# Kernel optimization log

Measured on AMD Instinct MI355X. Metric: run time of the kernel, lower is better.

Reference implementation:

```python
import jax, jax.numpy as jnp
import numpy as np

K = 100
TEMPERATURE = 0.1


def setup_inputs() -> dict:
    key = jax.random.key(0)
    k1, k2 = jax.random.split(key)
    x = jax.random.normal(k1, (8, 128, 60, 60), dtype=jnp.float32)
    W = jax.random.normal(k2, (128, 2 * K), dtype=jnp.float32) * 0.02  # torch Linear(k*2, d_model).weight
    b = jnp.zeros((128,), dtype=jnp.float32)
    return {"x": x, "W": W, "b": b}


def reference(x, W, b):
    x0, x1 = jnp.split(x, 2, axis=0)
    n, c, h, w = x0.shape
    hw = h * w
    # n c h w -> n (h w) c
    f0 = jnp.transpose(x0.reshape(n, c, hw), (0, 2, 1))
    f1 = jnp.transpose(x1.reshape(n, c, hw), (0, 2, 1))
    # (f0/sqrt(c)) @ (f1/sqrt(c))^T / T  ==  f0 @ f1^T / (c*T)
    sm = jnp.einsum('nld,nsd->nls', f0, f1) / (c * TEMPERATURE)
    cm = (jax.nn.softmax(sm, axis=1) * jax.nn.softmax(sm, axis=2)).reshape(n, hw * hw)
    _, topi = jax.lax.top_k(cm, K)  # (n, K)
    qindex = topi // hw
    rindex = topi % hw
    coords0 = jnp.stack([qindex % w, qindex // w], axis=-1).astype(jnp.float32) / w  # (n, K, 2) as (x, y)
    coords1 = jnp.stack([rindex % w, rindex // w], axis=-1).astype(jnp.float32) / w
    # create_meshgrid(h, w, normalized=False): (1, h*w, 2) with (x, y), row-major
    gy, gx = jnp.meshgrid(jnp.arange(h), jnp.arange(w), indexing='ij')
    grid = jnp.stack([gx, gy], axis=-1).reshape(1, hw, 2).astype(jnp.float32) / w
    offsets0 = grid[:, :, None, :] - coords0[:, None, :, :]  # (n, hw, K, 2)
    offsets1 = grid[:, :, None, :] - coords1[:, None, :, :]
    emb0 = offsets0.reshape(n, hw, 2 * K) @ W.T + b  # (n, hw, d_model)
    emb1 = offsets1.reshape(n, hw, 2 * K) @ W.T + b
    f0 = f0 + emb0
    f1 = f1 + emb1
    f = jnp.concatenate([f0, f1], axis=0)  # (2n, hw, d)
    # n (h w) d -> n d h w
    return jnp.transpose(f, (0, 2, 1)).reshape(2 * n, c, h, w)
```

## Files before the change

kernel.cpp:

```cpp
#include <hip/hip_runtime.h>

#define HW 3600
#define PADR 3712
#define NF4 900
#define CAP 16384
#define KSEL 100
#define NT 58
typedef unsigned long long U64;

using short8   = __attribute__((ext_vector_type(8))) short;
using float4v  = __attribute__((ext_vector_type(4))) float;
using float16v = __attribute__((ext_vector_type(16))) float;

__device__ __forceinline__ unsigned monof(float f) {
    unsigned b = __float_as_uint(f);
    return (b & 0x80000000u) ? ~b : (b | 0x80000000u);
}
__device__ __forceinline__ float unmonof(unsigned m) {
    return __uint_as_float((m & 0x80000000u) ? (m ^ 0x80000000u) : ~m);
}
__device__ __forceinline__ unsigned short f2bf(float f) {
    unsigned b = __float_as_uint(f);
    return (unsigned short)((b + 0x7FFFu + ((b >> 16) & 1u)) >> 16);
}
__device__ __forceinline__ float bf2f(unsigned short h) {
    return __uint_as_float(((unsigned)h) << 16);
}
__device__ __forceinline__ void async16(const void* g, void* l) {
    __builtin_amdgcn_global_load_lds((const __attribute__((address_space(1))) void*)g,
                                     (__attribute__((address_space(3))) void*)l, 16, 0, 0);
}


__global__ __launch_bounds__(256) void conv_k(
    const float* __restrict__ x,
    unsigned short* __restrict__ hiT, unsigned short* __restrict__ loT)
{
    int b = blockIdx.z, l0 = blockIdx.x * 64, d0 = blockIdx.y * 64;
    __shared__ float t[64][65];
    int tid = threadIdx.x;
#pragma unroll
    for (int r = 0; r < 4; r++) {
        int idx = tid + 256 * r;
        int d = idx >> 4, lq = idx & 15;
        int l = l0 + lq * 4;
        const float* src = x + ((size_t)b * 128 + d0 + d) * HW;
        float4 v;
        if (l + 3 < HW) v = *(const float4*)(src + l);
        else {
            v.x = (l     < HW) ? src[l]     : 0.f;
            v.y = (l + 1 < HW) ? src[l + 1] : 0.f;
            v.z = (l + 2 < HW) ? src[l + 2] : 0.f;
            v.w = (l + 3 < HW) ? src[l + 3] : 0.f;
        }
        t[lq * 4 + 0][d] = v.x; t[lq * 4 + 1][d] = v.y;
        t[lq * 4 + 2][d] = v.z; t[lq * 4 + 3][d] = v.w;
    }
    __syncthreads();
    const int rblk = l0 >> 7;
#pragma unroll
    for (int r = 0; r < 2; r++) {
        int idx = tid + 256 * r;
        int l = idx & 63, dq = idx >> 6;
        unsigned hp[4], lp[4];
#pragma unroll
        for (int j = 0; j < 4; j++) {
            float f0 = t[l][dq * 8 + 2 * j], f1 = t[l][dq * 8 + 2 * j + 1];
            unsigned short h0 = f2bf(f0), h1 = f2bf(f1);
            unsigned short g0 = f2bf(f0 - bf2f(h0)), g1 = f2bf(f1 - bf2f(h1));
            hp[j] = (unsigned)h0 | ((unsigned)h1 << 16);
            lp[j] = (unsigned)g0 | ((unsigned)g1 << 16);
        }
        size_t o = ((size_t)(b * 29 + rblk) * 16 + (d0 >> 3) + dq) * 1024
                 + (size_t)((l0 + l) & 127) * 8;
        *(uint4*)(hiT + o) = make_uint4(hp[0], hp[1], hp[2], hp[3]);
        *(uint4*)(loT + o) = make_uint4(lp[0], lp[1], lp[2], lp[3]);
    }
}

__global__ __launch_bounds__(256) void gemm_mfma_k(
    const unsigned short* __restrict__ hiT, const unsigned short* __restrict__ loT,
    float* __restrict__ den_row, float* __restrict__ den_col,
    float* __restrict__ maxvt)
{
    const int batch = blockIdx.z, bx = blockIdx.x, by = blockIdx.y;
    __shared__ __align__(16) unsigned char smem[34816];
    unsigned short (*stage)[4][128][8] = (unsigned short (*)[4][128][8])smem;

    const int tid = threadIdx.x;
    const int lane = tid & 63, w = tid >> 6;
    const int wr = w >> 1, wc = w & 1;
    const int l31 = lane & 31, h = lane >> 5;

    const unsigned short* psrc = (w == 0) ? hiT : (w == 1) ? loT : (w == 2) ? hiT : loT;
    const int bsel = (w < 2) ? batch : batch + 4;
    const int rblk = (w < 2) ? by : bx;
    const size_t cbase = ((size_t)(bsel * 29 + rblk) * 16) * 1024;

    float16v acc[2][2];
#pragma unroll
    for (int i = 0; i < 2; i++)
#pragma unroll
        for (int j = 0; j < 2; j++) acc[i][j] = (float16v)(0.f);

    for (int k0 = 0; k0 < 128; k0 += 32) {
#pragma unroll
        for (int i = 0; i < 8; i++) {
            int kb = i >> 1, half = i & 1;
            const unsigned short* g = psrc + cbase + (size_t)((k0 >> 3) + kb) * 1024
                                    + (half << 9) + lane * 8;
            async16(g, &stage[w][kb][half << 6][0]);
        }
        __syncthreads();
#pragma unroll
        for (int j = 0; j < 2; j++) {
            int kb = j * 2 + h;
            short8 ah[2], al[2], bh[2], bl[2];
#pragma unroll
            for (int t = 0; t < 2; t++) {
                ah[t] = *(const short8*)&stage[0][kb][wr * 64 + t * 32 + l31][0];
                al[t] = *(const short8*)&stage[1][kb][wr * 64 + t * 32 + l31][0];
                bh[t] = *(const short8*)&stage[2][kb][wc * 64 + t * 32 + l31][0];
                bl[t] = *(const short8*)&stage[3][kb][wc * 64 + t * 32 + l31][0];
            }
#pragma unroll
            for (int mt = 0; mt < 2; mt++)
#pragma unroll
                for (int nt = 0; nt < 2; nt++) {
                    acc[mt][nt] = __builtin_amdgcn_mfma_f32_32x32x16_bf16(ah[mt], bh[nt], acc[mt][nt], 0, 0, 0);
                    acc[mt][nt] = __builtin_amdgcn_mfma_f32_32x32x16_bf16(ah[mt], bl[nt], acc[mt][nt], 0, 0, 0);
                    acc[mt][nt] = __builtin_amdgcn_mfma_f32_32x32x16_bf16(al[mt], bh[nt], acc[mt][nt], 0, 0, 0);
                }
        }
        __syncthreads();
    }

    const float scale = 0.078125f;
    float* T = ((float*)smem) + w * (64 * 34);
    const bool interior = (bx < 28) && (by < 28);
    const int col0 = bx * 128 + wc * 64 + l31;
    const bool c0v = interior || (col0 < HW);
    const bool c1v = interior || (col0 + 32 < HW);
    float cs0 = 0.f, cs1 = 0.f;

#pragma unroll
    for (int mt = 0; mt < 2; mt++)
#pragma unroll
        for (int reg = 0; reg < 16; reg++) {
            float v0 = acc[mt][0][reg] * scale;
            float v1 = acc[mt][1][reg] * scale;
            float e0 = c0v ? __expf(v0) : 0.f;
            float e1 = c1v ? __expf(v1) : 0.f;
            int row64 = mt * 32 + (reg & 3) + 8 * (reg >> 2) + 4 * h;
            bool rv = interior || (by * 128 + wr * 64 + row64 < HW);
            if (rv) { cs0 += e0; cs1 += e1; }
            T[row64 * 34 + l31] = e0 + e1;
        }
    __asm__ __volatile__("s_waitcnt lgkmcnt(0)" ::: "memory");
    float rsum = 0.f;
#pragma unroll
    for (int i = 0; i < 16; i++) {
        float2 p = *(const float2*)&T[lane * 34 + 2 * i];
        rsum += p.x + p.y;
    }
    __asm__ __volatile__("s_waitcnt lgkmcnt(0)" ::: "memory");
    const int lrow = by * 128 + wr * 64 + lane;
    const bool rowv = interior || (lrow < HW);
    if (rowv) atomicAdd(&den_row[(size_t)batch * HW + lrow], rsum);

#pragma unroll
    for (int mt = 0; mt < 2; mt++)
#pragma unroll
        for (int reg = 0; reg < 16; reg++) {
            float m0 = c0v ? acc[mt][0][reg] : -3.4e38f;
            float m1 = c1v ? acc[mt][1][reg] : -3.4e38f;
            int row64 = mt * 32 + (reg & 3) + 8 * (reg >> 2) + 4 * h;
            T[row64 * 34 + l31] = fmaxf(m0, m1) * scale;
        }
    __asm__ __volatile__("s_waitcnt lgkmcnt(0)" ::: "memory");
    float rmax = -3.4e38f;
#pragma unroll
    for (int i = 0; i < 16; i++) {
        float2 p = *(const float2*)&T[lane * 34 + 2 * i];
        rmax = fmaxf(rmax, fmaxf(p.x, p.y));
    }
    const int ct = bx * 2 + wc;
    if (rowv) maxvt[((size_t)batch * NT + ct) * PADR + lrow] = rmax;

    cs0 += __shfl_xor(cs0, 32);
    cs1 += __shfl_xor(cs1, 32);
    if (h == 0) {
        if (c0v) atomicAdd(&den_col[(size_t)batch * HW + col0], cs0);
        if (c1v) atomicAdd(&den_col[(size_t)batch * HW + col0 + 32], cs1);
    }
}

__global__ __launch_bounds__(256) void stat_k(
    const float* __restrict__ den_row, const float* __restrict__ den_col,
    const float* __restrict__ maxvt, float* __restrict__ keylb)
{
    const int b = blockIdx.z, tid = threadIdx.x;
    __shared__ float lncS[HW];
    __shared__ float mlsS[NT];
    for (int i = tid; i < HW; i += 256)
        lncS[i] = __logf(den_col[(size_t)b * HW + i]);
    __syncthreads();
    if (tid < NT) {
        float mx = -3.4e38f;
        int s0 = tid * 64, s1 = s0 + 64; if (s1 > HW) s1 = HW;
        for (int s = s0; s < s1; s++) mx = fmaxf(mx, lncS[s]);
        if (s0 >= HW) mx = 1e30f;
        mlsS[tid] = mx;
    }
    __syncthreads();
    int j = blockIdx.x * 240 + tid;
    if (tid < 240 && j < HW) {
        float best = -3.4e38f;
#pragma unroll 2
        for (int t = 0; t < NT; t++)
            best = fmaxf(best, 2.0f * maxvt[((size_t)b * NT + t) * PADR + j] - mlsS[t]);
        keylb[(size_t)b * HW + j] = best - __logf(den_row[(size_t)b * HW + j]);
    }
}

__global__ __launch_bounds__(256) void tau_k(
    const float* __restrict__ keylb, float* __restrict__ tau)
{
    const int b = blockIdx.z, tid = threadIdx.x;
    __shared__ unsigned keyS[HW];
    __shared__ unsigned hist[4096];
    __shared__ unsigned pc[256];
    __shared__ int b1S, c1S, b2S, lcnt;
    __shared__ unsigned bestS;
    __shared__ unsigned list[1024];

    for (int i = tid; i < 4096; i += 256) hist[i] = 0u;
    if (tid == 0) { lcnt = 0; bestS = 0u; }
    __syncthreads();
    for (int i = tid; i < HW; i += 256) {
        unsigned k = monof(keylb[(size_t)b * HW + i]);
        keyS[i] = k;
        atomicAdd(&hist[k >> 20], 1u);
    }
    __syncthreads();
    { unsigned s = 0; for (int j = 0; j < 16; j++) s += hist[tid * 16 + j]; pc[tid] = s; }
    __syncthreads();
    if (tid == 0) {
        unsigned cum = 0; int cs_ = 255;
        for (; cs_ > 0; cs_--) { if (cum + pc[cs_] >= (unsigned)KSEL) break; cum += pc[cs_]; }
        int bb = cs_ * 16 + 15;
        for (; bb > cs_ * 16; bb--) { if (cum + hist[bb] >= (unsigned)KSEL) break; cum += hist[bb]; }
        b1S = bb; c1S = (int)cum;
    }
    __syncthreads();
    int b1 = b1S;
    for (int i = tid; i < 4096; i += 256) hist[i] = 0u;
    __syncthreads();
    for (int i = tid; i < HW; i += 256) {
        unsigned k = keyS[i];
        if ((int)(k >> 20) == b1) atomicAdd(&hist[(k >> 8) & 4095], 1u);
    }
    __syncthreads();
    { unsigned s = 0; for (int j = 0; j < 16; j++) s += hist[tid * 16 + j]; pc[tid] = s; }
    __syncthreads();
    if (tid == 0) {
        unsigned cum = (unsigned)c1S; int cs_ = 255;
        for (; cs_ > 0; cs_--) { if (cum + pc[cs_] >= (unsigned)KSEL) break; cum += pc[cs_]; }
        int bb = cs_ * 16 + 15;
        for (; bb > cs_ * 16; bb--) { if (cum + hist[bb] >= (unsigned)KSEL) break; cum += hist[bb]; }
        b2S = bb;
    }
    __syncthreads();
    int b2 = b2S;
    for (int i = tid; i < HW; i += 256) {
        unsigned k = keyS[i]; int hb = (int)(k >> 20);
        if (hb > b1 || (hb == b1 && (int)((k >> 8) & 4095) >= b2)) {
            int p = atomicAdd(&lcnt, 1);
            if (p < 1024) list[p] = k;
        }
    }
    __syncthreads();
    int L = lcnt; if (L > 1024) L = 1024;
    for (int i = tid; i < L; i += 256) {
        unsigned e = list[i]; int c = 0;
        for (int j = 0; j < L; j++) c += (list[j] >= e) ? 1 : 0;
        if (c >= KSEL) atomicMax(&bestS, e);
    }
    __syncthreads();
    if (tid == 0) tau[b] = unmonof(bestS) - 3e-4f;
}

__global__ __launch_bounds__(256) void recollect_k(
    const unsigned short* __restrict__ hiT, const unsigned short* __restrict__ loT,
    const float* __restrict__ den_row, const float* __restrict__ den_col,
    const float* __restrict__ maxvt, const float* __restrict__ tau,
    uint2* __restrict__ cand, int* __restrict__ cnt)
{
    const int t = blockIdx.x, batch = blockIdx.y;
    const int tid = threadIdx.x;
    __shared__ float lnrS[HW];
    __shared__ float lncS[64];
    __shared__ int prS[HW];
    __shared__ int pcS;
    __shared__ float mnlS;

    if (tid < 64) {
        int c = t * 64 + tid;
        float lc = (c < HW) ? __logf(den_col[(size_t)batch * HW + c]) : 1e30f;
        lncS[tid] = lc;
        float mn = lc;
#pragma unroll
        for (int off = 1; off < 64; off <<= 1) mn = fminf(mn, __shfl_xor(mn, off));
        if (tid == 0) mnlS = mn;
    }
    for (int r = tid; r < HW; r += 256)
        lnrS[r] = __logf(den_row[(size_t)batch * HW + r]);
    if (tid == 0) pcS = 0;
    __syncthreads();

    const float tv = tau[batch];
    const float tvm = tv - 3e-4f;
    const float mnl = mnlS;
    const float* mv = maxvt + ((size_t)batch * NT + t) * PADR;
    for (int r = tid; r < HW; r += 256) {
        float bnd = 2.0f * mv[r] - lnrS[r] - mnl;
        if (bnd >= tvm) {
            int p = atomicAdd(&pcS, 1);
            prS[p] = r;
        }
    }
    __syncthreads();
    const int pc = pcS;
    if (pc == 0) return;

    const unsigned short* Ah = hiT + 0;
    const unsigned short* Al = loT + 0;
    const int lane = tid & 63, w = tid >> 6;
    const int m = lane & 15, q = lane >> 4;
    const float scale = 0.078125f;
    const size_t abase = (size_t)batch * PADR * 128;
    const size_t bbase = (size_t)(batch + 4) * PADR * 128;

    for (int g = w; g * 16 < pc; g += 4) {
        int pi = g * 16 + m;
        int rowv = (pi < pc) ? prS[pi] : HW;
        float ldrv = (pi < pc) ? lnrS[rowv] : 0.f;
        size_t arow = abase + ((size_t)(rowv >> 7) * 16) * 1024 + (size_t)(rowv & 127) * 8;

        float4v acc[4];
#pragma unroll
        for (int i = 0; i < 4; i++) acc[i] = (float4v){0.f, 0.f, 0.f, 0.f};
#pragma unroll
        for (int k0 = 0; k0 < 128; k0 += 32) {
            int kb = (k0 >> 3) + q;
            short8 ah = *(const short8*)(Ah + arow + (size_t)kb * 1024);
            short8 al = *(const short8*)(Al + arow + (size_t)kb * 1024);
#pragma unroll
            for (int nt = 0; nt < 4; nt++) {
                int c = t * 64 + nt * 16 + m;
                size_t brow = bbase + ((size_t)(c >> 7) * 16 + kb) * 1024 + (size_t)(c & 127) * 8;
                short8 bh = *(const short8*)(hiT + brow);
                short8 bl = *(const short8*)(loT + brow);
                acc[nt] = __builtin_amdgcn_mfma_f32_16x16x32_bf16(ah, bh, acc[nt], 0, 0, 0);
                acc[nt] = __builtin_amdgcn_mfma_f32_16x16x32_bf16(ah, bl, acc[nt], 0, 0, 0);
                acc[nt] = __builtin_amdgcn_mfma_f32_16x16x32_bf16(al, bh, acc[nt], 0, 0, 0);
            }
        }
#pragma unroll
        for (int nt = 0; nt < 4; nt++) {
            int c = t * 64 + nt * 16 + m;
            if (c >= HW) continue;
            float ldc = lncS[nt * 16 + m];
#pragma unroll
            for (int r = 0; r < 4; r++) {
                int ri = q * 4 + r;
                if (g * 16 + ri >= pc) continue;
                int rowo = __shfl(rowv, ri);
                float ldro = __shfl(ldrv, ri);
                float v = acc[nt][r] * scale;
                float tt = 2.0f * v - ldro - ldc;
                if (tt >= tv) {
                    int p = atomicAdd(&cnt[batch], 1);
                    if (p < CAP)
                        cand[(size_t)batch * CAP + p] =
                            make_uint2(monof(tt), (unsigned)(rowo * HW + c));
                }
            }
        }
    }
}

__global__ __launch_bounds__(256) void select_k(
    const uint2* __restrict__ cand, const int* __restrict__ cnt,
    const float* __restrict__ W,
    float* __restrict__ C0, float* __restrict__ C1,
    float* __restrict__ Sx, float* __restrict__ Sy)
{
    const int batch = blockIdx.z, tid = threadIdx.x;
    const uint2* cb = cand + (size_t)batch * CAP;
    int M = cnt[batch]; if (M > CAP) M = CAP;

    __shared__ unsigned hist[4096];
    __shared__ unsigned pc[256];
    __shared__ int b1S, c1S, b2S, lcnt;
    __shared__ U64 list[512];
    __shared__ int topiS[KSEL];
    __shared__ float cx0S[KSEL], cy0S[KSEL], cx1S[KSEL], cy1S[KSEL];

    for (int i = tid; i < 4096; i += 256) hist[i] = 0u;
    if (tid == 0) lcnt = 0;
    __syncthreads();
    for (int i = tid; i < M; i += 256) atomicAdd(&hist[cb[i].x >> 20], 1u);
    __syncthreads();
    { unsigned s = 0; for (int j = 0; j < 16; j++) s += hist[tid * 16 + j]; pc[tid] = s; }
    __syncthreads();
    if (tid == 0) {
        unsigned cum = 0; int cs_ = 255;
        for (; cs_ > 0; cs_--) { if (cum + pc[cs_] >= (unsigned)KSEL) break; cum += pc[cs_]; }
        int bb = cs_ * 16 + 15;
        for (; bb > cs_ * 16; bb--) { if (cum + hist[bb] >= (unsigned)KSEL) break; cum += hist[bb]; }
        b1S = bb; c1S = (int)cum;
    }
    __syncthreads();
    int b1 = b1S;
    for (int i = tid; i < 4096; i += 256) hist[i] = 0u;
    __syncthreads();
    for (int i = tid; i < M; i += 256) {
        unsigned k = cb[i].x;
        if ((int)(k >> 20) == b1) atomicAdd(&hist[(k >> 8) & 4095], 1u);
    }
    __syncthreads();
    { unsigned s = 0; for (int j = 0; j < 16; j++) s += hist[tid * 16 + j]; pc[tid] = s; }
    __syncthreads();
    if (tid == 0) {
        unsigned cum = (unsigned)c1S; int cs_ = 255;
        for (; cs_ > 0; cs_--) { if (cum + pc[cs_] >= (unsigned)KSEL) break; cum += pc[cs_]; }
        int bb = cs_ * 16 + 15;
        for (; bb > cs_ * 16; bb--) { if (cum + hist[bb] >= (unsigned)KSEL) break; cum += hist[bb]; }
        b2S = bb;
    }
    __syncthreads();
    int b2 = b2S;
    for (int i = tid; i < M; i += 256) {
        uint2 e = cb[i];
        int hb = (int)(e.x >> 20);
        if (hb > b1 || (hb == b1 && (int)((e.x >> 8) & 4095) >= b2)) {
            int p = atomicAdd(&lcnt, 1);
            if (p < 512) list[p] = ((U64)e.x << 32) | (unsigned)(~e.y);
        }
    }
    __syncthreads();
    int L = lcnt; if (L > 512) L = 512;
    for (int i = tid; i < L; i += 256) {
        U64 e = list[i]; int r = 0;
        for (int j = 0; j < L; j++) r += (list[j] > e) ? 1 : 0;
        if (r < KSEL) topiS[r] = (int)(~(unsigned)(e & 0xffffffffu));
    }
    __syncthreads();

    if (tid < KSEL) {
        int idx = topiS[tid];
        int qq = idx / HW, rr = idx - qq * HW;
        cx0S[tid] = (float)(qq % 60) / 60.0f;
        cy0S[tid] = (float)(qq / 60) / 60.0f;
        cx1S[tid] = (float)(rr % 60) / 60.0f;
        cy1S[tid] = (float)(rr / 60) / 60.0f;
    }
    __syncthreads();
    if (tid < 128) {
        const float* wr_ = W + tid * 200;
        float c0 = 0.f, c1 = 0.f, sx = 0.f, sy = 0.f;
        for (int k = 0; k < KSEL; k++) {
            float wx = wr_[2 * k], wy = wr_[2 * k + 1];
            c0 += cx0S[k] * wx + cy0S[k] * wy;
            c1 += cx1S[k] * wx + cy1S[k] * wy;
            sx += wx; sy += wy;
        }
        C0[batch * 128 + tid] = c0;
        C1[batch * 128 + tid] = c1;
        if (batch == 0) { Sx[tid] = sx; Sy[tid] = sy; }
    }
}

__global__ __launch_bounds__(256) void final_k(
    const float* __restrict__ x, const float* __restrict__ bias,
    const float* __restrict__ C0, const float* __restrict__ C1,
    const float* __restrict__ Sx, const float* __restrict__ Sy,
    float* __restrict__ out)
{
    int bd = blockIdx.x;
    int b = bd >> 7, d = bd & 127;
    float cst = bias[d] - ((b < 4) ? C0[b * 128 + d] : C1[(b - 4) * 128 + d]);
    float sx = Sx[d], sy = Sy[d];
    const float4* xin = (const float4*)(x + (size_t)bd * HW);
    float4* o4 = (float4*)(out + (size_t)bd * HW);
    for (int f = threadIdx.x; f < NF4; f += 256) {
        float4 v = xin[f];
        int p0 = f * 4;
        float gy = (float)(p0 / 60) / 60.0f;
        float gxb = (float)(p0 % 60);
        float add = cst + gy * sy;
        v.x += add + ((gxb       ) / 60.0f) * sx;
        v.y += add + ((gxb + 1.f) / 60.0f) * sx;
        v.z += add + ((gxb + 2.f) / 60.0f) * sx;
        v.w += add + ((gxb + 3.f) / 60.0f) * sx;
        o4[f] = v;
    }
}

extern "C" void kernel_launch(void* const* d_in, const int* in_sizes, int n_in,
                              void* d_out, int out_size, void* d_ws, size_t ws_size,
                              hipStream_t stream)
{
    const float* x    = (const float*)d_in[0];
    const float* W    = (const float*)d_in[1];
    const float* bias = (const float*)d_in[2];
    float* out = (float*)d_out;

    char* ws = (char*)d_ws;
    float*    den_row = (float*)(ws + 0);
    float*    den_col = (float*)(ws + 57600);
    int*      cnt     = (int*)  (ws + 115200);
    float*    tau     = (float*)(ws + 115216);
    float*    keylb   = (float*)(ws + 115264);
    float*    C0      = (float*)(ws + 172864);
    float*    C1      = (float*)(ws + 174912);
    float*    Sx      = (float*)(ws + 176960);
    float*    Sy      = (float*)(ws + 177472);
    uint2*    cand    = (uint2*)(ws + 178048);
    float*    maxvt   = (float*)(ws + 702336);
    unsigned short* hiT = (unsigned short*)(ws + 4147072);
    unsigned short* loT = (unsigned short*)(ws + 11749248);

    hipMemsetAsync(ws, 0, 115232, stream);

    conv_k     <<<dim3(58, 2, 8),  256, 0, stream>>>(x, hiT, loT);
    gemm_mfma_k<<<dim3(29, 29, 4), 256, 0, stream>>>(hiT, loT, den_row, den_col, maxvt);
    stat_k     <<<dim3(15, 1, 4),  256, 0, stream>>>(den_row, den_col, maxvt, keylb);
    tau_k      <<<dim3(1, 1, 4),   256, 0, stream>>>(keylb, tau);
    recollect_k<<<dim3(NT, 4),     256, 0, stream>>>(hiT, loT, den_row, den_col, maxvt, tau, cand, cnt);
    select_k   <<<dim3(1, 1, 4),   256, 0, stream>>>(cand, cnt, W, C0, C1, Sx, Sy);
    final_k    <<<dim3(1024),      256, 0, stream>>>(x, bias, C0, C1, Sx, Sy, out);
}
```

Measured before the change: 229.9 us.

## Fuse stat/tau/select kernels, double-buffer GEMM stages, drop memset

The memset is replaced by zeroing the denominators inside conv_k. The GEMM now double-buffers its async LDS staging, waiting on vmcnt so the next k-slice loads while MFMAs run on the current one. The stat and tau computation is folded into every recollect_k block, each writing per-tile candidate slices without global atomics. Top-k selection plus the W projection are merged into final_k, which every output block recomputes redundantly. This cuts launches and serialized single-block kernels, at the cost of repeated threshold and top-k work per block and a 6144-entry candidate cap.

```diff
diff --git a/kernel.cpp b/kernel.cpp
--- a/kernel.cpp
+++ b/kernel.cpp
@@ -3,7 +3,7 @@
 #define HW 3600
 #define PADR 3712
 #define NF4 900
-#define CAP 16384
+#define SLICE 2048
 #define KSEL 100
 #define NT 58
 typedef unsigned long long U64;
@@ -34,11 +34,19 @@
 
 __global__ __launch_bounds__(256) void conv_k(
     const float* __restrict__ x,
-    unsigned short* __restrict__ hiT, unsigned short* __restrict__ loT)
+    unsigned short* __restrict__ hiT, unsigned short* __restrict__ loT,
+    float* __restrict__ den)
 {
     int b = blockIdx.z, l0 = blockIdx.x * 64, d0 = blockIdx.y * 64;
     __shared__ float t[64][65];
     int tid = threadIdx.x;
+    if (blockIdx.y == 0 && blockIdx.z == 0) {
+        int base = blockIdx.x * 512;
+        for (int i = tid; i < 512; i += 256) {
+            int g = base + i;
+            if (g < 28800) den[g] = 0.f;
+        }
+    }
 #pragma unroll
     for (int r = 0; r < 4; r++) {
         int idx = tid + 256 * r;
@@ -84,8 +92,7 @@
     float* __restrict__ maxvt)
 {
     const int batch = blockIdx.z, bx = blockIdx.x, by = blockIdx.y;
-    __shared__ __align__(16) unsigned char smem[34816];
-    unsigned short (*stage)[4][128][8] = (unsigned short (*)[4][128][8])smem;
+    __shared__ __align__(16) unsigned short stage[2][4][4][128][8];
 
     const int tid = threadIdx.x;
     const int lane = tid & 63, w = tid >> 6;
@@ -97,31 +104,43 @@
     const int rblk = (w < 2) ? by : bx;
     const size_t cbase = ((size_t)(bsel * 29 + rblk) * 16) * 1024;
 
-    float16v acc[2][2];
-#pragma unroll
-    for (int i = 0; i < 2; i++)
-#pragma unroll
-        for (int j = 0; j < 2; j++) acc[i][j] = (float16v)(0.f);
-
-    for (int k0 = 0; k0 < 128; k0 += 32) {
+    auto issue = [&](int buf, int k0) {
 #pragma unroll
         for (int i = 0; i < 8; i++) {
             int kb = i >> 1, half = i & 1;
             const unsigned short* g = psrc + cbase + (size_t)((k0 >> 3) + kb) * 1024
                                     + (half << 9) + lane * 8;
-            async16(g, &stage[w][kb][half << 6][0]);
-        }
-        __syncthreads();
+            async16(g, &stage[buf][w][kb][half << 6][0]);
+        }
+    };
+
+    float16v acc[2][2];
+#pragma unroll
+    for (int i = 0; i < 2; i++)
+#pragma unroll
+        for (int j = 0; j < 2; j++) acc[i][j] = (float16v)(0.f);
+
+    issue(0, 0);
+#pragma unroll
+    for (int it = 0; it < 4; it++) {
+        if (it < 3) {
+            issue((it + 1) & 1, (it + 1) * 32);
+            __asm__ __volatile__("s_waitcnt vmcnt(8)" ::: "memory");
+        } else {
+            __asm__ __volatile__("s_waitcnt vmcnt(0)" ::: "memory");
+        }
+        __asm__ __volatile__("s_barrier" ::: "memory");
+        const int cb = it & 1;
 #pragma unroll
         for (int j = 0; j < 2; j++) {
             int kb = j * 2 + h;
             short8 ah[2], al[2], bh[2], bl[2];
 #pragma unroll
             for (int t = 0; t < 2; t++) {
-                ah[t] = *(const short8*)&stage[0][kb][wr * 64 + t * 32 + l31][0];
-                al[t] = *(const short8*)&stage[1][kb][wr * 64 + t * 32 + l31][0];
-                bh[t] = *(const short8*)&stage[2][kb][wc * 64 + t * 32 + l31][0];
-                bl[t] = *(const short8*)&stage[3][kb][wc * 64 + t * 32 + l31][0];
+                ah[t] = *(const short8*)&stage[cb][0][kb][wr * 64 + t * 32 + l31][0];
+                al[t] = *(const short8*)&stage[cb][1][kb][wr * 64 + t * 32 + l31][0];
+                bh[t] = *(const short8*)&stage[cb][2][kb][wc * 64 + t * 32 + l31][0];
+                bl[t] = *(const short8*)&stage[cb][3][kb][wc * 64 + t * 32 + l31][0];
             }
 #pragma unroll
             for (int mt = 0; mt < 2; mt++)
@@ -132,11 +151,12 @@
                     acc[mt][nt] = __builtin_amdgcn_mfma_f32_32x32x16_bf16(al[mt], bh[nt], acc[mt][nt], 0, 0, 0);
                 }
         }
-        __syncthreads();
-    }
+        __asm__ __volatile__("s_barrier" ::: "memory");
+    }
+    __syncthreads();
 
     const float scale = 0.078125f;
-    float* T = ((float*)smem) + w * (64 * 34);
+    float* T = ((float*)stage) + w * (64 * 34);
     const bool interior = (bx < 28) && (by < 28);
     const int col0 = bx * 128 + wc * 64 + l31;
     const bool c0v = interior || (col0 < HW);
@@ -195,115 +215,33 @@
     }
 }
 
-__global__ __launch_bounds__(256) void stat_k(
-    const float* __restrict__ den_row, const float* __restrict__ den_col,
-    const float* __restrict__ maxvt, float* __restrict__ keylb)
-{
-    const int b = blockIdx.z, tid = threadIdx.x;
-    __shared__ float lncS[HW];
-    __shared__ float mlsS[NT];
-    for (int i = tid; i < HW; i += 256)
-        lncS[i] = __logf(den_col[(size_t)b * HW + i]);
-    __syncthreads();
-    if (tid < NT) {
-        float mx = -3.4e38f;
-        int s0 = tid * 64, s1 = s0 + 64; if (s1 > HW) s1 = HW;
-        for (int s = s0; s < s1; s++) mx = fmaxf(mx, lncS[s]);
-        if (s0 >= HW) mx = 1e30f;
-        mlsS[tid] = mx;
-    }
-    __syncthreads();
-    int j = blockIdx.x * 240 + tid;
-    if (tid < 240 && j < HW) {
-        float best = -3.4e38f;
-#pragma unroll 2
-        for (int t = 0; t < NT; t++)
-            best = fmaxf(best, 2.0f * maxvt[((size_t)b * NT + t) * PADR + j] - mlsS[t]);
-        keylb[(size_t)b * HW + j] = best - __logf(den_row[(size_t)b * HW + j]);
-    }
-}
-
-__global__ __launch_bounds__(256) void tau_k(
-    const float* __restrict__ keylb, float* __restrict__ tau)
-{
-    const int b = blockIdx.z, tid = threadIdx.x;
-    __shared__ unsigned keyS[HW];
-    __shared__ unsigned hist[4096];
-    __shared__ unsigned pc[256];
-    __shared__ int b1S, c1S, b2S, lcnt;
-    __shared__ unsigned bestS;
-    __shared__ unsigned list[1024];
-
-    for (int i = tid; i < 4096; i += 256) hist[i] = 0u;
-    if (tid == 0) { lcnt = 0; bestS = 0u; }
-    __syncthreads();
-    for (int i = tid; i < HW; i += 256) {
-        unsigned k = monof(keylb[(size_t)b * HW + i]);
-        keyS[i] = k;
-        atomicAdd(&hist[k >> 20], 1u);
-    }
-    __syncthreads();
-    { unsigned s = 0; for (int j = 0; j < 16; j++) s += hist[tid * 16 + j]; pc[tid] = s; }
-    __syncthreads();
-    if (tid == 0) {
-        unsigned cum = 0; int cs_ = 255;
-        for (; cs_ > 0; cs_--) { if (cum + pc[cs_] >= (unsigned)KSEL) break; cum += pc[cs_]; }
-        int bb = cs_ * 16 + 15;
-        for (; bb > cs_ * 16; bb--) { if (cum + hist[bb] >= (unsigned)KSEL) break; cum += hist[bb]; }
-        b1S = bb; c1S = (int)cum;
-    }
-    __syncthreads();
-    int b1 = b1S;
-    for (int i = tid; i < 4096; i += 256) hist[i] = 0u;
-    __syncthreads();
-    for (int i = tid; i < HW; i += 256) {
-        unsigned k = keyS[i];
-        if ((int)(k >> 20) == b1) atomicAdd(&hist[(k >> 8) & 4095], 1u);
-    }
-    __syncthreads();
-    { unsigned s = 0; for (int j = 0; j < 16; j++) s += hist[tid * 16 + j]; pc[tid] = s; }
-    __syncthreads();
-    if (tid == 0) {
-        unsigned cum = (unsigned)c1S; int cs_ = 255;
-        for (; cs_ > 0; cs_--) { if (cum + pc[cs_] >= (unsigned)KSEL) break; cum += pc[cs_]; }
-        int bb = cs_ * 16 + 15;
-        for (; bb > cs_ * 16; bb--) { if (cum + hist[bb] >= (unsigned)KSEL) break; cum += hist[bb]; }
-        b2S = bb;
-    }
-    __syncthreads();
-    int b2 = b2S;
-    for (int i = tid; i < HW; i += 256) {
-        unsigned k = keyS[i]; int hb = (int)(k >> 20);
-        if (hb > b1 || (hb == b1 && (int)((k >> 8) & 4095) >= b2)) {
-            int p = atomicAdd(&lcnt, 1);
-            if (p < 1024) list[p] = k;
-        }
-    }
-    __syncthreads();
-    int L = lcnt; if (L > 1024) L = 1024;
-    for (int i = tid; i < L; i += 256) {
-        unsigned e = list[i]; int c = 0;
-        for (int j = 0; j < L; j++) c += (list[j] >= e) ? 1 : 0;
-        if (c >= KSEL) atomicMax(&bestS, e);
-    }
-    __syncthreads();
-    if (tid == 0) tau[b] = unmonof(bestS) - 3e-4f;
-}
-
 __global__ __launch_bounds__(256) void recollect_k(
     const unsigned short* __restrict__ hiT, const unsigned short* __restrict__ loT,
     const float* __restrict__ den_row, const float* __restrict__ den_col,
-    const float* __restrict__ maxvt, const float* __restrict__ tau,
-    uint2* __restrict__ cand, int* __restrict__ cnt)
+    const float* __restrict__ maxvt,
+    uint2* __restrict__ cand, int* __restrict__ cnt58)
 {
     const int t = blockIdx.x, batch = blockIdx.y;
     const int tid = threadIdx.x;
     __shared__ float lnrS[HW];
+    __shared__ float maxlncS[NT];
     __shared__ float lncS[64];
-    __shared__ int prS[HW];
-    __shared__ int pcS;
-    __shared__ float mnlS;
-
+    __shared__ float mnlS, tauS;
+    __shared__ unsigned uS[HW];
+    __shared__ unsigned hist[4096];
+    __shared__ unsigned hpc[256];
+    __shared__ int b1S, c1S, b2S, lcntS, pcS, ccS;
+    __shared__ unsigned bestS;
+    __shared__ unsigned listS[1024];
+
+    for (int i = tid; i < HW; i += 256)
+        lnrS[i] = __logf(den_row[(size_t)batch * HW + i]);
+    if (tid < NT) {
+        float mx = -3.4e38f;
+        int s0 = tid * 64, s1 = s0 + 64; if (s1 > HW) s1 = HW;
+        for (int s = s0; s < s1; s++) mx = fmaxf(mx, __logf(den_col[(size_t)batch * HW + s]));
+        maxlncS[tid] = (s0 < HW) ? mx : 1e30f;
+    }
     if (tid < 64) {
         int c = t * 64 + tid;
         float lc = (c < HW) ? __logf(den_col[(size_t)batch * HW + c]) : 1e30f;
@@ -313,12 +251,67 @@
         for (int off = 1; off < 64; off <<= 1) mn = fminf(mn, __shfl_xor(mn, off));
         if (tid == 0) mnlS = mn;
     }
-    for (int r = tid; r < HW; r += 256)
-        lnrS[r] = __logf(den_row[(size_t)batch * HW + r]);
-    if (tid == 0) pcS = 0;
-    __syncthreads();
-
-    const float tv = tau[batch];
+    for (int i = tid; i < 4096; i += 256) hist[i] = 0u;
+    if (tid == 0) { lcntS = 0; bestS = 0u; pcS = 0; ccS = 0; }
+    __syncthreads();
+
+    for (int r = tid; r < HW; r += 256) {
+        float best = -3.4e38f;
+        for (int tt = 0; tt < NT; tt++)
+            best = fmaxf(best, 2.0f * maxvt[((size_t)batch * NT + tt) * PADR + r] - maxlncS[tt]);
+        unsigned k = monof(best - lnrS[r]);
+        uS[r] = k;
+        atomicAdd(&hist[k >> 20], 1u);
+    }
+    __syncthreads();
+    { unsigned s = 0; for (int j = 0; j < 16; j++) s += hist[tid * 16 + j]; hpc[tid] = s; }
+    __syncthreads();
+    if (tid == 0) {
+        unsigned cum = 0; int cs_ = 255;
+        for (; cs_ > 0; cs_--) { if (cum + hpc[cs_] >= (unsigned)KSEL) break; cum += hpc[cs_]; }
+        int bb = cs_ * 16 + 15;
+        for (; bb > cs_ * 16; bb--) { if (cum + hist[bb] >= (unsigned)KSEL) break; cum += hist[bb]; }
+        b1S = bb; c1S = (int)cum;
+    }
+    __syncthreads();
+    int b1 = b1S;
+    for (int i = tid; i < 4096; i += 256) hist[i] = 0u;
+    __syncthreads();
+    for (int i = tid; i < HW; i += 256) {
+        unsigned k = uS[i];
+        if ((int)(k >> 20) == b1) atomicAdd(&hist[(k >> 8) & 4095], 1u);
+    }
+    __syncthreads();
+    { unsigned s = 0; for (int j = 0; j < 16; j++) s += hist[tid * 16 + j]; hpc[tid] = s; }
+    __syncthreads();
+    if (tid == 0) {
+        unsigned cum = (unsigned)c1S; int cs_ = 255;
+        for (; cs_ > 0; cs_--) { if (cum + hpc[cs_] >= (unsigned)KSEL) break; cum += hpc[cs_]; }
+        int bb = cs_ * 16 + 15;
+        for (; bb > cs_ * 16; bb--) { if (cum + hist[bb] >= (unsigned)KSEL) break; cum += hist[bb]; }
+        b2S = bb;
+    }
+    __syncthreads();
+    int b2 = b2S;
+    for (int i = tid; i < HW; i += 256) {
+        unsigned k = uS[i]; int hb = (int)(k >> 20);
+        if (hb > b1 || (hb == b1 && (int)((k >> 8) & 4095) >= b2)) {
+            int p = atomicAdd(&lcntS, 1);
+            if (p < 1024) listS[p] = k;
+        }
+    }
+    __syncthreads();
+    int L = lcntS; if (L > 1024) L = 1024;
+    for (int i = tid; i < L; i += 256) {
+        unsigned e = listS[i]; int c = 0;
+        for (int j = 0; j < L; j++) c += (listS[j] >= e) ? 1 : 0;
+        if (c >= KSEL) atomicMax(&bestS, e);
+    }
+    __syncthreads();
+    if (tid == 0) tauS = unmonof(bestS) - 3e-4f;
+    __syncthreads();
+
+    const float tv = tauS;
     const float tvm = tv - 3e-4f;
     const float mnl = mnlS;
     const float* mv = maxvt + ((size_t)batch * NT + t) * PADR;
@@ -326,175 +319,153 @@
         float bnd = 2.0f * mv[r] - lnrS[r] - mnl;
         if (bnd >= tvm) {
             int p = atomicAdd(&pcS, 1);
-            prS[p] = r;
+            ((int*)uS)[p] = r;
         }
     }
     __syncthreads();
     const int pc = pcS;
-    if (pc == 0) return;
-
-    const unsigned short* Ah = hiT + 0;
-    const unsigned short* Al = loT + 0;
-    const int lane = tid & 63, w = tid >> 6;
-    const int m = lane & 15, q = lane >> 4;
-    const float scale = 0.078125f;
-    const size_t abase = (size_t)batch * PADR * 128;
-    const size_t bbase = (size_t)(batch + 4) * PADR * 128;
-
-    for (int g = w; g * 16 < pc; g += 4) {
-        int pi = g * 16 + m;
-        int rowv = (pi < pc) ? prS[pi] : HW;
-        float ldrv = (pi < pc) ? lnrS[rowv] : 0.f;
-        size_t arow = abase + ((size_t)(rowv >> 7) * 16) * 1024 + (size_t)(rowv & 127) * 8;
-
-        float4v acc[4];
-#pragma unroll
-        for (int i = 0; i < 4; i++) acc[i] = (float4v){0.f, 0.f, 0.f, 0.f};
-#pragma unroll
-        for (int k0 = 0; k0 < 128; k0 += 32) {
-            int kb = (k0 >> 3) + q;
-            short8 ah = *(const short8*)(Ah + arow + (size_t)kb * 1024);
-            short8 al = *(const short8*)(Al + arow + (size_t)kb * 1024);
+    uint2* candS = (uint2*)hist;
+
+    if (pc > 0) {
+        const int* pr = (const int*)uS;
+        const int lane = tid & 63, w = tid >> 6;
+        const int m = lane & 15, q = lane >> 4;
+        const float scale = 0.078125f;
+        const size_t abase = (size_t)batch * PADR * 128;
+        const size_t bbase = (size_t)(batch + 4) * PADR * 128;
+
+        for (int g = w; g * 16 < pc; g += 4) {
+            int pi = g * 16 + m;
+            int rowv = (pi < pc) ? pr[pi] : HW;
+            float ldrv = (pi < pc) ? lnrS[rowv] : 0.f;
+            size_t arow = abase + ((size_t)(rowv >> 7) * 16) * 1024 + (size_t)(rowv & 127) * 8;
+
+            float4v acc[4];
+#pragma unroll
+            for (int i = 0; i < 4; i++) acc[i] = (float4v){0.f, 0.f, 0.f, 0.f};
+#pragma unroll
+            for (int k0 = 0; k0 < 128; k0 += 32) {
+                int kb = (k0 >> 3) + q;
+                short8 ah = *(const short8*)(hiT + arow + (size_t)kb * 1024);
+                short8 al = *(const short8*)(loT + arow + (size_t)kb * 1024);
+#pragma unroll
+                for (int nt = 0; nt < 4; nt++) {
+                    int c = t * 64 + nt * 16 + m;
+                    size_t brow = bbase + ((size_t)(c >> 7) * 16 + kb) * 1024 + (size_t)(c & 127) * 8;
+                    short8 bh = *(const short8*)(hiT + brow);
+                    short8 bl = *(const short8*)(loT + brow);
+                    acc[nt] = __builtin_amdgcn_mfma_f32_16x16x32_bf16(ah, bh, acc[nt], 0, 0, 0);
+                    acc[nt] = __builtin_amdgcn_mfma_f32_16x16x32_bf16(ah, bl, acc[nt], 0, 0, 0);
+                    acc[nt] = __builtin_amdgcn_mfma_f32_16x16x32_bf16(al, bh, acc[nt], 0, 0, 0);
+                }
+            }
 #pragma unroll
             for (int nt = 0; nt < 4; nt++) {
                 int c = t * 64 + nt * 16 + m;
-                size_t brow = bbase + ((size_t)(c >> 7) * 16 + kb) * 1024 + (size_t)(c & 127) * 8;
-                short8 bh = *(const short8*)(hiT + brow);
-                short8 bl = *(const short8*)(loT + brow);
-                acc[nt] = __builtin_amdgcn_mfma_f32_16x16x32_bf16(ah, bh, acc[nt], 0, 0, 0);
-                acc[nt] = __builtin_amdgcn_mfma_f32_16x16x32_bf16(ah, bl, acc[nt], 0, 0, 0);
-                acc[nt] = __builtin_amdgcn_mfma_f32_16x16x32_bf16(al, bh, acc[nt], 0, 0, 0);
-            }
-        }
-#pragma unroll
-        for (int nt = 0; nt < 4; nt++) {
-            int c = t * 64 + nt * 16 + m;
-            if (c >= HW) continue;
-            float ldc = lncS[nt * 16 + m];
-#pragma unroll
-            for (int r = 0; r < 4; r++) {
-                int ri = q * 4 + r;
-                if (g * 16 + ri >= pc) continue;
-                int rowo = __shfl(rowv, ri);
-                float ldro = __shfl(ldrv, ri);
-                float v = acc[nt][r] * scale;
-                float tt = 2.0f * v - ldro - ldc;
-                if (tt >= tv) {
-                    int p = atomicAdd(&cnt[batch], 1);
-                    if (p < CAP)
-                        cand[(size_t)batch * CAP + p] =
-                            make_uint2(monof(tt), (unsigned)(rowo * HW + c));
+                if (c >= HW) continue;
+                float ldc = lncS[nt * 16 + m];
+#pragma unroll
+                for (int r = 0; r < 4; r++) {
+                    int ri = q * 4 + r;
+                    if (g * 16 + ri >= pc) continue;
+                    int rowo = __shfl(rowv, ri);
+                    float ldro = __shfl(ldrv, ri);
+                    float v = acc[nt][r] * scale;
+                    float tt2 = 2.0f * v - ldro - ldc;
+                    if (tt2 >= tv) {
+                        int p = atomicAdd(&ccS, 1);
+                        if (p < SLICE)
+                            candS[p] = make_uint2(monof(tt2), (unsigned)(rowo * HW + c));
+                    }
                 }
             }
         }
     }
-}
-
-__global__ __launch_bounds__(256) void select_k(
-    const uint2* __restrict__ cand, const int* __restrict__ cnt,
-    const float* __restrict__ W,
-    float* __restrict__ C0, float* __restrict__ C1,
-    float* __restrict__ Sx, float* __restrict__ Sy)
+    __syncthreads();
+    int cc = ccS; if (cc > SLICE) cc = SLICE;
+    uint2* slice = cand + ((size_t)batch * NT + t) * SLICE;
+    for (int i = tid; i < cc; i += 256) slice[i] = candS[i];
+    if (tid == 0) cnt58[batch * NT + t] = cc;
+}
+
+__global__ __launch_bounds__(256) void final_k(
+    const float* __restrict__ x, const float* __restrict__ W,
+    const float* __restrict__ bias,
+    const uint2* __restrict__ cand, const int* __restrict__ cnt58,
+    float* __restrict__ out)
 {
-    const int batch = blockIdx.z, tid = threadIdx.x;
-    const uint2* cb = cand + (size_t)batch * CAP;
-    int M = cnt[batch]; if (M > CAP) M = CAP;
-
-    __shared__ unsigned hist[4096];
-    __shared__ unsigned pc[256];
-    __shared__ int b1S, c1S, b2S, lcnt;
-    __shared__ U64 list[512];
+    const int bd = blockIdx.x;
+    const int b8 = bd >> 7, d = bd & 127;
+    const int batch = b8 & 3;
+    const bool useQ = (b8 < 4);
+    const int tid = threadIdx.x;
+    const int lane = tid & 63, w = tid >> 6;
+
+    __shared__ U64 lk[6144];
+    __shared__ int offS[NT + 1];
     __shared__ int topiS[KSEL];
-    __shared__ float cx0S[KSEL], cy0S[KSEL], cx1S[KSEL], cy1S[KSEL];
-
-    for (int i = tid; i < 4096; i += 256) hist[i] = 0u;
-    if (tid == 0) lcnt = 0;
-    __syncthreads();
-    for (int i = tid; i < M; i += 256) atomicAdd(&hist[cb[i].x >> 20], 1u);
-    __syncthreads();
-    { unsigned s = 0; for (int j = 0; j < 16; j++) s += hist[tid * 16 + j]; pc[tid] = s; }
-    __syncthreads();
+    __shared__ float cxS[KSEL], cyS[KSEL];
+    __shared__ float redC[4], redX[4], redY[4];
+    __shared__ float cstS, sxS, syS;
+
     if (tid == 0) {
-        unsigned cum = 0; int cs_ = 255;
-        for (; cs_ > 0; cs_--) { if (cum + pc[cs_] >= (unsigned)KSEL) break; cum += pc[cs_]; }
-        int bb = cs_ * 16 + 15;
-        for (; bb > cs_ * 16; bb--) { if (cum + hist[bb] >= (unsigned)KSEL) break; cum += hist[bb]; }
-        b1S = bb; c1S = (int)cum;
-    }
-    __syncthreads();
-    int b1 = b1S;
-    for (int i = tid; i < 4096; i += 256) hist[i] = 0u;
+        int o = 0;
+        for (int t = 0; t < NT; t++) {
+            offS[t] = o;
+            o += cnt58[batch * NT + t];
+            if (o > 6144) o = 6144;
+        }
+        offS[NT] = o;
+    }
+    __syncthreads();
+    const int M = offS[NT];
+    for (int t = 0; t < NT; t++) {
+        int o0 = offS[t], n = offS[t + 1] - o0;
+        const uint2* slice = cand + ((size_t)batch * NT + t) * SLICE;
+        for (int i = tid; i < n; i += 256) {
+            uint2 e = slice[i];
+            lk[o0 + i] = ((U64)e.x << 32) | (unsigned)(~e.y);
+        }
+    }
     __syncthreads();
     for (int i = tid; i < M; i += 256) {
-        unsigned k = cb[i].x;
-        if ((int)(k >> 20) == b1) atomicAdd(&hist[(k >> 8) & 4095], 1u);
-    }
-    __syncthreads();
-    { unsigned s = 0; for (int j = 0; j < 16; j++) s += hist[tid * 16 + j]; pc[tid] = s; }
-    __syncthreads();
-    if (tid == 0) {
-        unsigned cum = (unsigned)c1S; int cs_ = 255;
-        for (; cs_ > 0; cs_--) { if (cum + pc[cs_] >= (unsigned)KSEL) break; cum += pc[cs_]; }
-        int bb = cs_ * 16 + 15;
-        for (; bb > cs_ * 16; bb--) { if (cum + hist[bb] >= (unsigned)KSEL) break; cum += hist[bb]; }
-        b2S = bb;
-    }
-    __syncthreads();
-    int b2 = b2S;
-    for (int i = tid; i < M; i += 256) {
-        uint2 e = cb[i];
-        int hb = (int)(e.x >> 20);
-        if (hb > b1 || (hb == b1 && (int)((e.x >> 8) & 4095) >= b2)) {
-            int p = atomicAdd(&lcnt, 1);
-            if (p < 512) list[p] = ((U64)e.x << 32) | (unsigned)(~e.y);
-        }
-    }
-    __syncthreads();
-    int L = lcnt; if (L > 512) L = 512;
-    for (int i = tid; i < L; i += 256) {
-        U64 e = list[i]; int r = 0;
-        for (int j = 0; j < L; j++) r += (list[j] > e) ? 1 : 0;
+        U64 e = lk[i]; int r = 0;
+        for (int j = 0; j < M; j++) r += (lk[j] > e) ? 1 : 0;
         if (r < KSEL) topiS[r] = (int)(~(unsigned)(e & 0xffffffffu));
     }
     __syncthreads();
-
     if (tid < KSEL) {
         int idx = topiS[tid];
         int qq = idx / HW, rr = idx - qq * HW;
-        cx0S[tid] = (float)(qq % 60) / 60.0f;
-        cy0S[tid] = (float)(qq / 60) / 60.0f;
-        cx1S[tid] = (float)(rr % 60) / 60.0f;
-        cy1S[tid] = (float)(rr / 60) / 60.0f;
-    }
-    __syncthreads();
-    if (tid < 128) {
-        const float* wr_ = W + tid * 200;
-        float c0 = 0.f, c1 = 0.f, sx = 0.f, sy = 0.f;
-        for (int k = 0; k < KSEL; k++) {
-            float wx = wr_[2 * k], wy = wr_[2 * k + 1];
-            c0 += cx0S[k] * wx + cy0S[k] * wy;
-            c1 += cx1S[k] * wx + cy1S[k] * wy;
-            sx += wx; sy += wy;
-        }
-        C0[batch * 128 + tid] = c0;
-        C1[batch * 128 + tid] = c1;
-        if (batch == 0) { Sx[tid] = sx; Sy[tid] = sy; }
-    }
-}
-
-__global__ __launch_bounds__(256) void final_k(
-    const float* __restrict__ x, const float* __restrict__ bias,
-    const float* __restrict__ C0, const float* __restrict__ C1,
-    const float* __restrict__ Sx, const float* __restrict__ Sy,
-    float* __restrict__ out)
-{
-    int bd = blockIdx.x;
-    int b = bd >> 7, d = bd & 127;
-    float cst = bias[d] - ((b < 4) ? C0[b * 128 + d] : C1[(b - 4) * 128 + d]);
-    float sx = Sx[d], sy = Sy[d];
+        int sel = useQ ? qq : rr;
+        cxS[tid] = (float)(sel % 60) / 60.0f;
+        cyS[tid] = (float)(sel / 60) / 60.0f;
+    }
+    __syncthreads();
+    float pC = 0.f, pX = 0.f, pY = 0.f;
+    if (tid < KSEL) {
+        float wx = W[d * 200 + 2 * tid], wy = W[d * 200 + 2 * tid + 1];
+        pC = cxS[tid] * wx + cyS[tid] * wy;
+        pX = wx; pY = wy;
+    }
+#pragma unroll
+    for (int off = 1; off < 64; off <<= 1) {
+        pC += __shfl_xor(pC, off);
+        pX += __shfl_xor(pX, off);
+        pY += __shfl_xor(pY, off);
+    }
+    if (lane == 0) { redC[w] = pC; redX[w] = pX; redY[w] = pY; }
+    __syncthreads();
+    if (tid == 0) {
+        cstS = bias[d] - (redC[0] + redC[1] + redC[2] + redC[3]);
+        sxS  = redX[0] + redX[1] + redX[2] + redX[3];
+        syS  = redY[0] + redY[1] + redY[2] + redY[3];
+    }
+    __syncthreads();
+    const float cst = cstS, sx = sxS, sy = syS;
     const float4* xin = (const float4*)(x + (size_t)bd * HW);
     float4* o4 = (float4*)(out + (size_t)bd * HW);
-    for (int f = threadIdx.x; f < NF4; f += 256) {
+    for (int f = tid; f < NF4; f += 256) {
         float4 v = xin[f];
         int p0 = f * 4;
         float gy = (float)(p0 / 60) / 60.0f;
@@ -518,27 +489,17 @@
     float* out = (float*)d_out;
 
     char* ws = (char*)d_ws;
-    float*    den_row = (float*)(ws + 0);
+    float*    den     = (float*)(ws + 0);
+    float*    den_row = den;
     float*    den_col = (float*)(ws + 57600);
-    int*      cnt     = (int*)  (ws + 115200);
-    float*    tau     = (float*)(ws + 115216);
-    float*    keylb   = (float*)(ws + 115264);
-    float*    C0      = (float*)(ws + 172864);
-    float*    C1      = (float*)(ws + 174912);
-    float*    Sx      = (float*)(ws + 176960);
-    float*    Sy      = (float*)(ws + 177472);
-    uint2*    cand    = (uint2*)(ws + 178048);
-    float*    maxvt   = (float*)(ws + 702336);
-    unsigned short* hiT = (unsigned short*)(ws + 4147072);
-    unsigned short* loT = (unsigned short*)(ws + 11749248);
-
-    hipMemsetAsync(ws, 0, 115232, stream);
-
-    conv_k     <<<dim3(58, 2, 8),  256, 0, stream>>>(x, hiT, loT);
+    int*      cnt58   = (int*)  (ws + 115200);
+    uint2*    cand    = (uint2*)(ws + 116224);
+    float*    maxvt   = (float*)(ws + 3917312);
+    unsigned short* hiT = (unsigned short*)(ws + 7362048);
+    unsigned short* loT = (unsigned short*)(ws + 14964224);
+
+    conv_k     <<<dim3(58, 2, 8),  256, 0, stream>>>(x, hiT, loT, den);
     gemm_mfma_k<<<dim3(29, 29, 4), 256, 0, stream>>>(hiT, loT, den_row, den_col, maxvt);
-    stat_k     <<<dim3(15, 1, 4),  256, 0, stream>>>(den_row, den_col, maxvt, keylb);
-    tau_k      <<<dim3(1, 1, 4),   256, 0, stream>>>(keylb, tau);
-    recollect_k<<<dim3(NT, 4),     256, 0, stream>>>(hiT, loT, den_row, den_col, maxvt, tau, cand, cnt);
-    select_k   <<<dim3(1, 1, 4),   256, 0, stream>>>(cand, cnt, W, C0, C1, Sx, Sy);
-    final_k    <<<dim3(1024),      256, 0, stream>>>(x, bias, C0, C1, Sx, Sy, out);
-}
+    recollect_k<<<dim3(NT, 4),     256, 0, stream>>>(hiT, loT, den_row, den_col, maxvt, cand, cnt58);
+    final_k    <<<dim3(1024),      256, 0, stream>>>(x, W, bias, cand, cnt58, out);
+}
```

Measured after the change: 349.8 us. +52.2%, slower.
